# Kernel tuning notes

Measured on AMD Instinct MI355X. Metric: run time of the kernel, lower is better.

Reference implementation:

```python
import jax, jax.numpy as jnp
import numpy as np

B, S, D = 4, 2048, 64
H = 16            # num_heads
HD = D // H       # head_dim = 4 (code's misnamed 'num_heads' variable)
EPS = 1e-5        # BatchNorm1d default eps


def setup_inputs() -> dict:
    key = jax.random.key(0)
    ks = jax.random.split(key, 8)
    sc = 1.0 / np.sqrt(D)
    return {
        "x": jax.random.normal(ks[0], (B, S, D), dtype=jnp.float32),
        "Wq": jax.random.normal(ks[1], (D, D), dtype=jnp.float32) * sc,
        "bq": jnp.zeros((D,), dtype=jnp.float32),
        "Wk": jax.random.normal(ks[2], (D, D), dtype=jnp.float32) * sc,
        "bk": jnp.zeros((D,), dtype=jnp.float32),
        "Wv": jax.random.normal(ks[3], (D, D), dtype=jnp.float32) * sc,
        "bv": jnp.zeros((D,), dtype=jnp.float32),
        "gamma": jnp.ones((D,), dtype=jnp.float32),
        "beta": jnp.zeros((D,), dtype=jnp.float32),
    }


def reference(x, Wq, bq, Wk, bk, Wv, bv, gamma, beta):
    # ReLU-activated QKV projections
    Q = jax.nn.relu(jnp.einsum("bsd,de->bse", x, Wq) + bq)
    K = jax.nn.relu(jnp.einsum("bsd,de->bse", x, Wk) + bk)
    V = jax.nn.relu(jnp.einsum("bsd,de->bse", x, Wv) + bv)

    # split(dim=2)->cat(dim=0) is equivalent to head-split reshape [B,S,H,HD]
    Qh = Q.reshape(B, S, H, HD)
    Kh = K.reshape(B, S, H, HD)
    Vh = V.reshape(B, S, H, HD)

    scores = jnp.einsum("bqhd,bkhd->bhqk", Qh, Kh) / jnp.sqrt(jnp.float32(HD))
    attn = jax.nn.softmax(scores, axis=-1)  # dropout_rate = 0.0 -> no-op
    out = jnp.einsum("bhqk,bkhd->bqhd", attn, Vh).reshape(B, S, D)

    # residual
    out = out + x

    # BatchNorm1d(64) in training mode: batch stats over (B, S) per channel
    mean = jnp.mean(out, axis=(0, 1))
    var = jnp.var(out, axis=(0, 1))  # biased variance, as used for normalization
    out = (out - mean) * jax.lax.rsqrt(var + EPS) * gamma + beta
    return out
```

## Files before the change

### kernel.cpp

```cpp
#include <hip/hip_runtime.h>

#define BB 4
#define SS 2048
#define DD 64
#define HH 16
#define HDD 4
#define NBH (BB*HH)
#define NROWS (BB*SS)
#define NQ (NBH*SS)
#define QTILES 8
#define LOG2E_HALF 0.7213475204444817f

typedef float f32x2 __attribute__((ext_vector_type(2)));

__global__ __launch_bounds__(256) void qkv_kernel(
    const float* __restrict__ x,
    const float* __restrict__ Wq, const float* __restrict__ bq,
    const float* __restrict__ Wk, const float* __restrict__ bk,
    const float* __restrict__ Wv, const float* __restrict__ bv,
    float* __restrict__ Q, float* __restrict__ KV)
{
    __shared__ float xs[4 * 64];
    const int tid = threadIdx.x;
    const int row0 = blockIdx.x * 4;

    xs[tid] = x[(size_t)row0 * 64 + tid];
    __syncthreads();

    const int r = tid >> 6;
    const int c = tid & 63;
    const int row = row0 + r;
    const int b = row >> 11;
    const int s = row & (SS - 1);
    const float* xr = &xs[r * 64];

    float aq = bq[c], ak = bk[c], av = bv[c];
    #pragma unroll 16
    for (int k = 0; k < 64; ++k) {
        const float xv = xr[k];
        aq = fmaf(xv, Wq[k * 64 + c], aq);
        ak = fmaf(xv, Wk[k * 64 + c], ak);
        av = fmaf(xv, Wv[k * 64 + c], av);
    }
    aq = fmaxf(aq, 0.0f);
    ak = fmaxf(ak, 0.0f) * LOG2E_HALF;
    av = fmaxf(av, 0.0f);

    const int h = c >> 2, hd = c & 3;
    const size_t bhs = ((size_t)(b * HH + h) * SS + s);
    Q[bhs * 4 + hd] = aq;

    const int p = s >> 1, po = s & 1;
    const size_t pb = ((size_t)(b * HH + h) * (SS / 2) + p) * 16;
    KV[pb + hd * 2 + po] = ak;
    KV[pb + 8 + hd * 2 + po] = av;
}

template<int KSPLIT, int QROWS, bool DIRECT>
__global__ __launch_bounds__(256) void attn_kernel(
    const float* __restrict__ Qb, const float* __restrict__ KVb,
    const float* __restrict__ x, float* __restrict__ y,
    float* __restrict__ accS, float* __restrict__ sumS)
{
    constexpr int QT = SS / (256 * QROWS);
    constexpr int PAIRS = SS / 2 / KSPLIT;
    __shared__ float4 kvs4[PAIRS * 4];
    const f32x2* kvs = (const f32x2*)kvs4;

    const int tid = threadIdx.x;
    int blk = blockIdx.x;
    const int ks = blk / (NBH * QT);
    blk -= ks * (NBH * QT);
    const int bh = blk / QT;
    const int qt = blk - bh * QT;

    const float4* kvg = (const float4*)(KVb + ((size_t)bh * (SS / 2) + (size_t)ks * PAIRS) * 16);
    #pragma unroll
    for (int i = 0; i < PAIRS * 4 / 256; ++i)
        kvs4[i * 256 + tid] = kvg[i * 256 + tid];

    f32x2 qx[QROWS], qy[QROWS], qz[QROWS], qw[QROWS];
    #pragma unroll
    for (int r = 0; r < QROWS; ++r) {
        const int qrow = qt * (256 * QROWS) + r * 256 + tid;
        const float4 q = ((const float4*)Qb)[(size_t)bh * SS + qrow];
        qx[r] = {q.x, q.x}; qy[r] = {q.y, q.y};
        qz[r] = {q.z, q.z}; qw[r] = {q.w, q.w};
    }

    f32x2 acx[QROWS], acy[QROWS], acz[QROWS], acw[QROWS], sm[QROWS];
    #pragma unroll
    for (int r = 0; r < QROWS; ++r) {
        acx[r] = {0.f, 0.f}; acy[r] = {0.f, 0.f};
        acz[r] = {0.f, 0.f}; acw[r] = {0.f, 0.f};
        sm[r] = {0.f, 0.f};
    }

    __syncthreads();

    #pragma unroll 2
    for (int j = 0; j < PAIRS; ++j) {
        const f32x2 kx = kvs[j * 8 + 0];
        const f32x2 ky = kvs[j * 8 + 1];
        const f32x2 kz = kvs[j * 8 + 2];
        const f32x2 kw = kvs[j * 8 + 3];
        const f32x2 vx = kvs[j * 8 + 4];
        const f32x2 vy = kvs[j * 8 + 5];
        const f32x2 vz = kvs[j * 8 + 6];
        const f32x2 vw = kvs[j * 8 + 7];
        #pragma unroll
        for (int r = 0; r < QROWS; ++r) {
            f32x2 s = qx[r] * kx;
            s = __builtin_elementwise_fma(qy[r], ky, s);
            s = __builtin_elementwise_fma(qz[r], kz, s);
            s = __builtin_elementwise_fma(qw[r], kw, s);
            f32x2 e;
            e.x = __builtin_amdgcn_exp2f(s.x);
            e.y = __builtin_amdgcn_exp2f(s.y);
            sm[r] += e;
            acx[r] = __builtin_elementwise_fma(e, vx, acx[r]);
            acy[r] = __builtin_elementwise_fma(e, vy, acy[r]);
            acz[r] = __builtin_elementwise_fma(e, vz, acz[r]);
            acw[r] = __builtin_elementwise_fma(e, vw, acw[r]);
        }
    }

    #pragma unroll
    for (int r = 0; r < QROWS; ++r) {
        const int qrow = qt * (256 * QROWS) + r * 256 + tid;
        const float sum = sm[r].x + sm[r].y;
        float4 acc = {acx[r].x + acx[r].y, acy[r].x + acy[r].y,
                      acz[r].x + acz[r].y, acw[r].x + acw[r].y};
        if (DIRECT) {
            const float inv = 1.0f / sum;
            const int b = bh >> 4, h = bh & 15;
            const size_t o = ((size_t)(b * SS + qrow)) * DD + h * HDD;
            const float4 xr = *(const float4*)(x + o);
            float4 out;
            out.x = fmaf(acc.x, inv, xr.x);
            out.y = fmaf(acc.y, inv, xr.y);
            out.z = fmaf(acc.z, inv, xr.z);
            out.w = fmaf(acc.w, inv, xr.w);
            *(float4*)(y + o) = out;
        } else {
            const size_t qi = (size_t)ks * NQ + (size_t)bh * SS + qrow;
            ((float4*)accS)[qi] = acc;
            sumS[qi] = sum;
        }
    }
}

template<int KSPLIT>
__global__ __launch_bounds__(256) void combine_bn(
    const float* __restrict__ accS, const float* __restrict__ sumS,
    const float* __restrict__ x, float* __restrict__ y,
    float* __restrict__ part2)
{
    __shared__ float r[4][8];
    const int tid = threadIdx.x;
    const int bh = blockIdx.x >> 3;
    const int qt = blockIdx.x & 7;
    const int qrow = qt * 256 + tid;
    const size_t qi = (size_t)bh * SS + qrow;

    float4 a = ((const float4*)accS)[qi];
    float s = sumS[qi];
    #pragma unroll
    for (int k = 1; k < KSPLIT; ++k) {
        const float4 a2 = ((const float4*)accS)[(size_t)k * NQ + qi];
        a.x += a2.x; a.y += a2.y; a.z += a2.z; a.w += a2.w;
        s += sumS[(size_t)k * NQ + qi];
    }
    const float inv = 1.0f / s;
    const int b = bh >> 4, h = bh & 15;
    const size_t o = ((size_t)(b * SS + qrow)) * DD + h * HDD;
    const float4 xr = *(const float4*)(x + o);
    float4 out;
    out.x = fmaf(a.x, inv, xr.x);
    out.y = fmaf(a.y, inv, xr.y);
    out.z = fmaf(a.z, inv, xr.z);
    out.w = fmaf(a.w, inv, xr.w);
    *(float4*)(y + o) = out;

    float v[8] = {out.x, out.y, out.z, out.w,
                  out.x * out.x, out.y * out.y, out.z * out.z, out.w * out.w};
    #pragma unroll
    for (int i = 0; i < 8; ++i) {
        float t = v[i];
        for (int off = 32; off > 0; off >>= 1) t += __shfl_down(t, off);
        v[i] = t;
    }
    const int wid = tid >> 6;
    if ((tid & 63) == 0) {
        #pragma unroll
        for (int i = 0; i < 8; ++i) r[wid][i] = v[i];
    }
    __syncthreads();
    if (tid < 8) {
        const float t = r[0][tid] + r[1][tid] + r[2][tid] + r[3][tid];
        const int slot = b * 8 + qt;
        const int i = tid & 3;
        const int c = h * 4 + i;
        if (tid < 4) part2[c * 32 + slot] = t;
        else         part2[2048 + c * 32 + slot] = t;
    }
}

__global__ __launch_bounds__(256) void bn_norm_fused(
    float* __restrict__ y, const float* __restrict__ part2,
    const float* __restrict__ gamma, const float* __restrict__ beta)
{
    __shared__ float st[128];
    const int tid = threadIdx.x;
    if (tid < 128) {
        const int c = tid & 63;
        const float* p = part2 + (tid >> 6) * 2048 + c * 32;
        float s = 0.f;
        #pragma unroll
        for (int i = 0; i < 32; ++i) s += p[i];
        st[tid] = s;
    }
    __syncthreads();

    const int idx = blockIdx.x * 256 + tid;
    const int c0 = (idx & 15) * 4;
    float4 v = ((const float4*)y)[idx];
    const float n = 1.0f / NROWS;
    const float m0 = st[c0] * n,     m1 = st[c0 + 1] * n;
    const float m2 = st[c0 + 2] * n, m3 = st[c0 + 3] * n;
    const float r0 = rsqrtf(st[64 + c0] * n - m0 * m0 + 1e-5f);
    const float r1 = rsqrtf(st[65 + c0] * n - m1 * m1 + 1e-5f);
    const float r2 = rsqrtf(st[66 + c0] * n - m2 * m2 + 1e-5f);
    const float r3 = rsqrtf(st[67 + c0] * n - m3 * m3 + 1e-5f);
    float4 o;
    o.x = fmaf((v.x - m0) * r0, gamma[c0],     beta[c0]);
    o.y = fmaf((v.y - m1) * r1, gamma[c0 + 1], beta[c0 + 1]);
    o.z = fmaf((v.z - m2) * r2, gamma[c0 + 2], beta[c0 + 2]);
    o.w = fmaf((v.w - m3) * r3, gamma[c0 + 3], beta[c0 + 3]);
    ((float4*)y)[idx] = o;
}

__global__ __launch_bounds__(256) void bn_reduce1(
    const float* __restrict__ y, float* __restrict__ part)
{
    __shared__ float ls[256], ls2[256];
    const int tid = threadIdx.x;
    const int c = tid & 63;
    const int rg = tid >> 6;
    const int row0 = blockIdx.x * 32 + rg * 8;
    float s = 0.0f, s2 = 0.0f;
    #pragma unroll
    for (int i = 0; i < 8; ++i) {
        const float v = y[(size_t)(row0 + i) * 64 + c];
        s += v;
        s2 = fmaf(v, v, s2);
    }
    ls[tid] = s; ls2[tid] = s2;
    __syncthreads();
    if (rg == 0) {
        part[blockIdx.x * 64 + c] = ls[c] + ls[64 + c] + ls[128 + c] + ls[192 + c];
        part[256 * 64 + blockIdx.x * 64 + c] = ls2[c] + ls2[64 + c] + ls2[128 + c] + ls2[192 + c];
    }
}

__global__ __launch_bounds__(256) void bn_reduce2(
    const float* __restrict__ part, float* __restrict__ stats)
{
    __shared__ float ls[256], ls2[256];
    const int tid = threadIdx.x;
    const int c = tid & 63;
    const int pg = tid >> 6;
    float s = 0.0f, s2 = 0.0f;
    for (int i = pg; i < 256; i += 4) {
        s  += part[i * 64 + c];
        s2 += part[256 * 64 + i * 64 + c];
    }
    ls[tid] = s; ls2[tid] = s2;
    __syncthreads();
    if (pg == 0) {
        const float ts  = ls[c]  + ls[64 + c]  + ls[128 + c]  + ls[192 + c];
        const float ts2 = ls2[c] + ls2[64 + c] + ls2[128 + c] + ls2[192 + c];
        const float mean = ts * (1.0f / NROWS);
        const float var  = ts2 * (1.0f / NROWS) - mean * mean;
        stats[c] = mean;
        stats[64 + c] = rsqrtf(var + 1e-5f);
    }
}

__global__ __launch_bounds__(256) void bn_norm(
    float* __restrict__ y, const float* __restrict__ stats,
    const float* __restrict__ gamma, const float* __restrict__ beta)
{
    const int idx = blockIdx.x * 256 + threadIdx.x;
    const int c = idx & 63;
    const float v = y[idx];
    y[idx] = fmaf((v - stats[c]) * stats[64 + c], gamma[c], beta[c]);
}

extern "C" void kernel_launch(void* const* d_in, const int* in_sizes, int n_in,
                              void* d_out, int out_size, void* d_ws, size_t ws_size,
                              hipStream_t stream)
{
    const float* x     = (const float*)d_in[0];
    const float* Wq    = (const float*)d_in[1];
    const float* bq    = (const float*)d_in[2];
    const float* Wk    = (const float*)d_in[3];
    const float* bk    = (const float*)d_in[4];
    const float* Wv    = (const float*)d_in[5];
    const float* bv    = (const float*)d_in[6];
    const float* gamma = (const float*)d_in[7];
    const float* beta  = (const float*)d_in[8];
    float* out = (float*)d_out;

    float* ws = (float*)d_ws;
    float* Q  = ws;
    float* KV = ws + 524288;

    qkv_kernel<<<NROWS / 4, 256, 0, stream>>>(x, Wq, bq, Wk, bk, Wv, bv, Q, KV);

    const size_t base = 524288 + 1048576;
    auto need = [](int kk) {
        return (size_t)(524288 + 1048576 + (size_t)kk * NQ * 5 + 4096 + 128) * 4;
    };
    constexpr int QR = 2;
    constexpr int QT = SS / (256 * QR);

    if (ws_size >= need(8)) {
        float* accS  = ws + base;
        float* sumS  = accS + (size_t)8 * NQ * 4;
        float* part2 = sumS + (size_t)8 * NQ;
        attn_kernel<8, QR, false><<<8 * NBH * QT, 256, 0, stream>>>(Q, KV, x, out, accS, sumS);
        combine_bn<8><<<NBH * QTILES, 256, 0, stream>>>(accS, sumS, x, out, part2);
        bn_norm_fused<<<NROWS * DD / 1024, 256, 0, stream>>>(out, part2, gamma, beta);
    } else if (ws_size >= need(4)) {
        float* accS  = ws + base;
        float* sumS  = accS + (size_t)4 * NQ * 4;
        float* part2 = sumS + (size_t)4 * NQ;
        attn_kernel<4, QR, false><<<4 * NBH * QT, 256, 0, stream>>>(Q, KV, x, out, accS, sumS);
        combine_bn<4><<<NBH * QTILES, 256, 0, stream>>>(accS, sumS, x, out, part2);
        bn_norm_fused<<<NROWS * DD / 1024, 256, 0, stream>>>(out, part2, gamma, beta);
    } else if (ws_size >= need(2)) {
        float* accS  = ws + base;
        float* sumS  = accS + (size_t)2 * NQ * 4;
        float* part2 = sumS + (size_t)2 * NQ;
        attn_kernel<2, QR, false><<<2 * NBH * QT, 256, 0, stream>>>(Q, KV, x, out, accS, sumS);
        combine_bn<2><<<NBH * QTILES, 256, 0, stream>>>(accS, sumS, x, out, part2);
        bn_norm_fused<<<NROWS * DD / 1024, 256, 0, stream>>>(out, part2, gamma, beta);
    } else {
        float* part  = ws + base;
        float* stats = part + 32768;
        attn_kernel<1, QR, true><<<NBH * QT, 256, 0, stream>>>(Q, KV, x, out, nullptr, nullptr);
        bn_reduce1<<<256, 256, 0, stream>>>(out, part);
        bn_reduce2<<<1, 256, 0, stream>>>(part, stats);
        bn_norm<<<NROWS * DD / 256, 256, 0, stream>>>(out, stats, gamma, beta);
    }
}
```

Measured before the change: 111.1 us.

## Fuse split-K combine and BatchNorm normalize with a grid-wide barrier

Replaces the separate combine_bn and bn_norm_fused kernels with one kernel that merges the split-K partials, writes per-block channel statistics, waits on a global atomic counter until all 512 blocks have arrived, then reduces the statistics and writes the normalized output directly. This removes a kernel launch and the write and re-read of the intermediate output tensor. It adds a memset per call and relies on all 512 blocks being resident at the same time, which risks deadlock if occupancy is insufficient.

After: 165.3 us. 1.49x slower.

```diff
diff --git a/kernel.cpp b/kernel.cpp
--- a/kernel.cpp
+++ b/kernel.cpp
@@ -9,6 +9,7 @@
 #define NROWS (BB*SS)
 #define NQ (NBH*SS)
 #define QTILES 8
+#define CNBLK (NBH*QTILES)
 #define LOG2E_HALF 0.7213475204444817f
 
 typedef float f32x2 __attribute__((ext_vector_type(2)));
@@ -151,6 +152,98 @@
 }
 
 template<int KSPLIT>
+__global__ __launch_bounds__(256, 2) void combine_bn_norm(
+    const float* __restrict__ accS, const float* __restrict__ sumS,
+    const float* __restrict__ x, float* __restrict__ y,
+    float* __restrict__ part2, unsigned int* __restrict__ counter,
+    const float* __restrict__ gamma, const float* __restrict__ beta)
+{
+    __shared__ float rr[4][8];
+    __shared__ float st8[8];
+    const int tid = threadIdx.x;
+    const int bh = blockIdx.x >> 3;
+    const int qt = blockIdx.x & 7;
+    const int qrow = qt * 256 + tid;
+    const size_t qi = (size_t)bh * SS + qrow;
+
+    float4 a = ((const float4*)accS)[qi];
+    float s = sumS[qi];
+    #pragma unroll
+    for (int k = 1; k < KSPLIT; ++k) {
+        const float4 a2 = ((const float4*)accS)[(size_t)k * NQ + qi];
+        a.x += a2.x; a.y += a2.y; a.z += a2.z; a.w += a2.w;
+        s += sumS[(size_t)k * NQ + qi];
+    }
+    const float inv = 1.0f / s;
+    const int b = bh >> 4, h = bh & 15;
+    const size_t o = ((size_t)(b * SS + qrow)) * DD + h * HDD;
+    const float4 xr = *(const float4*)(x + o);
+    float4 out;
+    out.x = fmaf(a.x, inv, xr.x);
+    out.y = fmaf(a.y, inv, xr.y);
+    out.z = fmaf(a.z, inv, xr.z);
+    out.w = fmaf(a.w, inv, xr.w);
+
+    float v[8] = {out.x, out.y, out.z, out.w,
+                  out.x * out.x, out.y * out.y, out.z * out.z, out.w * out.w};
+    #pragma unroll
+    for (int i = 0; i < 8; ++i) {
+        float t = v[i];
+        for (int off = 32; off > 0; off >>= 1) t += __shfl_down(t, off);
+        v[i] = t;
+    }
+    const int wid = tid >> 6;
+    if ((tid & 63) == 0) {
+        #pragma unroll
+        for (int i = 0; i < 8; ++i) rr[wid][i] = v[i];
+    }
+    __syncthreads();
+    if (tid < 8) {
+        const float t = rr[0][tid] + rr[1][tid] + rr[2][tid] + rr[3][tid];
+        const int slot = b * 8 + qt;
+        const int i = tid & 3;
+        const int c = h * 4 + i;
+        float* dst = (tid < 4) ? &part2[c * 32 + slot]
+                               : &part2[2048 + c * 32 + slot];
+        __hip_atomic_store(dst, t, __ATOMIC_RELAXED, __HIP_MEMORY_SCOPE_AGENT);
+    }
+    __threadfence();
+    __syncthreads();
+
+    if (tid == 0) {
+        __hip_atomic_fetch_add(counter, 1u, __ATOMIC_ACQ_REL, __HIP_MEMORY_SCOPE_AGENT);
+        while (__hip_atomic_load(counter, __ATOMIC_ACQUIRE, __HIP_MEMORY_SCOPE_AGENT) < (unsigned)CNBLK)
+            __builtin_amdgcn_s_sleep(32);
+    }
+    __syncthreads();
+
+    {
+        const int sel = tid >> 5;
+        const int reg = sel >> 2;
+        const int ci  = h * 4 + (sel & 3);
+        float pv = __hip_atomic_load(&part2[reg * 2048 + ci * 32 + (tid & 31)],
+                                     __ATOMIC_RELAXED, __HIP_MEMORY_SCOPE_AGENT);
+        #pragma unroll
+        for (int off = 16; off > 0; off >>= 1) pv += __shfl_down(pv, off, 32);
+        if ((tid & 31) == 0) st8[sel] = pv;
+    }
+    __syncthreads();
+
+    const float n = 1.0f / NROWS;
+    const int c0 = h * 4;
+    const float m0 = st8[0] * n, m1 = st8[1] * n, m2 = st8[2] * n, m3 = st8[3] * n;
+    const float r0 = rsqrtf(st8[4] * n - m0 * m0 + 1e-5f);
+    const float r1 = rsqrtf(st8[5] * n - m1 * m1 + 1e-5f);
+    const float r2 = rsqrtf(st8[6] * n - m2 * m2 + 1e-5f);
+    const float r3 = rsqrtf(st8[7] * n - m3 * m3 + 1e-5f);
+    out.x = fmaf((out.x - m0) * r0, gamma[c0],     beta[c0]);
+    out.y = fmaf((out.y - m1) * r1, gamma[c0 + 1], beta[c0 + 1]);
+    out.z = fmaf((out.z - m2) * r2, gamma[c0 + 2], beta[c0 + 2]);
+    out.w = fmaf((out.w - m3) * r3, gamma[c0 + 3], beta[c0 + 3]);
+    *(float4*)(y + o) = out;
+}
+
+template<int KSPLIT>
 __global__ __launch_bounds__(256) void combine_bn(
     const float* __restrict__ accS, const float* __restrict__ sumS,
     const float* __restrict__ x, float* __restrict__ y,
@@ -329,9 +422,10 @@
         float* accS  = ws + base;
         float* sumS  = accS + (size_t)8 * NQ * 4;
         float* part2 = sumS + (size_t)8 * NQ;
+        unsigned int* counter = (unsigned int*)(part2 + 4096);
+        hipMemsetAsync(counter, 0, sizeof(unsigned int), stream);
         attn_kernel<8, QR, false><<<8 * NBH * QT, 256, 0, stream>>>(Q, KV, x, out, accS, sumS);
-        combine_bn<8><<<NBH * QTILES, 256, 0, stream>>>(accS, sumS, x, out, part2);
-        bn_norm_fused<<<NROWS * DD / 1024, 256, 0, stream>>>(out, part2, gamma, beta);
+        combine_bn_norm<8><<<CNBLK, 256, 0, stream>>>(accS, sumS, x, out, part2, counter, gamma, beta);
     } else if (ws_size >= need(4)) {
         float* accS  = ws + base;
         float* sumS  = accS + (size_t)4 * NQ * 4;
```
